# Optimization experiments

Measured on AMD Instinct MI355X. Metric: run time of the kernel, lower is better.

Reference implementation:

```python
import jax, jax.numpy as jnp
import numpy as np

K = 5
TAU = 0.5
N = 8192
IN_DIM = 128
OUT_DIM = 128


def setup_inputs() -> dict:
    key = jax.random.key(0)
    k1, k2, k3 = jax.random.split(key, 3)
    x = jax.random.normal(k1, (N, IN_DIM), dtype=jnp.float32)
    laplacian = jax.random.normal(k2, (N, N), dtype=jnp.float32) / np.sqrt(N)
    # xavier-uniform-like init for theta (K, in_dim, out_dim)
    limit = np.sqrt(6.0 / (IN_DIM + OUT_DIM))
    theta = jax.random.uniform(k3, (K, IN_DIM, OUT_DIM), dtype=jnp.float32,
                               minval=-limit, maxval=limit)
    return {"x": x, "laplacian": laplacian, "theta": theta}


def _cheb_coeff(k_order: int, tau: float) -> jnp.ndarray:
    # c_k = (2/K) * exp(-tau * cos(pi*(k+0.5)/K)), Chebyshev-Gauss nodes
    ks = jnp.arange(k_order, dtype=jnp.float32)
    x_k = jnp.cos(jnp.pi * (ks + 0.5) / k_order)
    return (2.0 / k_order) * jnp.exp(-tau * x_k)


def reference(x, laplacian, theta):
    coeff = _cheb_coeff(K, TAU)  # (K,)
    # Chebyshev recurrence: T_0 = x, T_1 = L x, T_k = 2 L T_{k-1} - T_{k-2}
    tx_prev, tx_curr = x, laplacian @ x
    tx_list = [tx_prev, tx_curr]
    for _ in range(2, K):
        tx_next = 2.0 * (laplacian @ tx_curr) - tx_prev
        tx_list.append(tx_next)
        tx_prev, tx_curr = tx_curr, tx_next
    tx_stack = jnp.stack(tx_list, axis=0)  # (K, N, in_dim)
    return jnp.einsum('kni,kio,k->no', tx_stack, theta, coeff)
```

## Files before the change

### kernel.cpp

```cpp
#include <hip/hip_runtime.h>
#include <hip/hip_bf16.h>
#include <cmath>

#define NROWS 8192
#define DIM   128
#define KDIM  8192
#define BM    32
#define BN    128
#define BK    64
#define SPLITK 4
#define KCHUNK (KDIM / SPLITK)
#define GITERS (KCHUNK / BK)
#define MTILES (NROWS / BM)
#define LDSTRIDE 80

typedef __bf16 bf16_t;
typedef __bf16 bf16x8 __attribute__((ext_vector_type(8)));
typedef float  f32x4  __attribute__((ext_vector_type(4)));

__device__ __forceinline__ void async16(const void* g, void* l) {
    __builtin_amdgcn_global_load_lds(
        (const __attribute__((address_space(1))) unsigned int*)g,
        (__attribute__((address_space(3))) unsigned int*)l, 16, 0, 0);
}

__global__ void k_theta(const float* __restrict__ th, bf16_t* __restrict__ out,
                        float c0, float c1, float c2, float c3, float c4) {
    int idx = blockIdx.x * 256 + threadIdx.x;
    int k = idx >> 14;
    int o = (idx >> 7) & 127;
    int i = idx & 127;
    float c = (k == 0) ? c0 : (k == 1) ? c1 : (k == 2) ? c2 : (k == 3) ? c3 : c4;
    out[idx] = (bf16_t)(c * th[(k << 14) + (i << 7) + o]);
}

template <int MODE>
__global__ __launch_bounds__(256, 4)
void k_gemm(const void* __restrict__ Ap, const bf16_t* __restrict__ Bt,
            float* __restrict__ partial, bf16_t* __restrict__ Lbf_out) {
    __shared__ __align__(16) bf16_t As[2][BM * BK];
    __shared__ __align__(16) bf16_t Bs[2][BN * BK];

    const int t     = threadIdx.x;
    const int mTile = blockIdx.x & (MTILES - 1);
    const int s     = blockIdx.x >> 8;
    const int mb    = mTile * BM;
    const int k0base = s * KCHUNK;
    const int wave = t >> 6, lane = t & 63;
    const int wM = (wave & 1) * 16;
    const int wN = (wave >> 1) * 64;
    const int lm = lane & 15, lk = lane >> 4;
    const int lrow = lane >> 3;
    const int lsrc = (lane & 7) ^ lrow;
    const int rA   = wave * 8 + lrow;

    f32x4 acc[4];
#pragma unroll
    for (int b = 0; b < 4; ++b) acc[b] = (f32x4)0.0f;

    float4 RA[2][2];

    auto stageB = [&](int kk, int buf) {
        const int k0 = k0base + kk * BK;
#pragma unroll
        for (int i = 0; i < 4; ++i) {
            const int n = wave * 32 + i * 8 + lrow;
            async16(Bt + (size_t)n * KDIM + k0 + lsrc * 8,
                    &Bs[buf][(wave * 32 + i * 8) * BK]);
        }
    };
    auto stageA0 = [&](int kk, int buf) {
        const int k0 = k0base + kk * BK;
        async16((const bf16_t*)Ap + (size_t)(mb + rA) * KDIM + k0 + lsrc * 8,
                &As[buf][wave * 8 * BK]);
    };
    auto loadA2 = [&](int kk, int p) {
        const int k0 = k0base + kk * BK;
        const float* base = (const float*)Ap + (size_t)(mb + rA) * KDIM + k0 + lsrc * 8;
        RA[p][0] = *(const float4*)base;
        RA[p][1] = *(const float4*)(base + 4);
    };
    auto writeA2 = [&](int kk, int buf, int p) {
        bf16x8 v;
        v[0] = (bf16_t)RA[p][0].x; v[1] = (bf16_t)RA[p][0].y;
        v[2] = (bf16_t)RA[p][0].z; v[3] = (bf16_t)RA[p][0].w;
        v[4] = (bf16_t)RA[p][1].x; v[5] = (bf16_t)RA[p][1].y;
        v[6] = (bf16_t)RA[p][1].z; v[7] = (bf16_t)RA[p][1].w;
        *(bf16x8*)(&As[buf][rA * BK + (lane & 7) * 8]) = v;
        const int k0 = k0base + kk * BK;
        *(bf16x8*)(Lbf_out + (size_t)(mb + rA) * KDIM + k0 + lsrc * 8) = v;
    };

    auto compute = [&](int buf) {
#pragma unroll
        for (int ko = 0; ko < 2; ++ko) {
            const int csX = (ko * 4 + lk) ^ (lm & 7);
            bf16x8 af = *(const bf16x8*)(&As[buf][(wM + lm) * BK + csX * 8]);
            bf16x8 bfr[4];
#pragma unroll
            for (int tn = 0; tn < 4; ++tn)
                bfr[tn] = *(const bf16x8*)(&Bs[buf][(wN + tn * 16 + lm) * BK + csX * 8]);
#pragma unroll
            for (int tn = 0; tn < 4; ++tn)
                acc[tn] = __builtin_amdgcn_mfma_f32_16x16x32_bf16(
                    af, bfr[tn], acc[tn], 0, 0, 0);
        }
    };

    if (MODE == 0) {
        stageA0(0, 0); stageB(0, 0);
        for (int kk = 0; kk < GITERS; ++kk) {
            const int buf = kk & 1;
            __syncthreads();
            if (kk + 1 < GITERS) { stageA0(kk + 1, buf ^ 1); stageB(kk + 1, buf ^ 1); }
            compute(buf);
        }
    } else {
        loadA2(0, 0); stageB(0, 0);
        for (int kk = 0; kk < GITERS; ++kk) {
            const int buf = kk & 1;
            writeA2(kk, buf, kk & 1);
            __syncthreads();
            if (kk + 1 < GITERS) { loadA2(kk + 1, (kk + 1) & 1); stageB(kk + 1, buf ^ 1); }
            compute(buf);
        }
    }

    float* pOut = partial + (size_t)s * NROWS * DIM;
#pragma unroll
    for (int tn = 0; tn < 4; ++tn)
#pragma unroll
        for (int r = 0; r < 4; ++r) {
            const int row = mb + wM + lk * 4 + r;
            const int col = wN + tn * 16 + lm;
            pOut[(size_t)row * DIM + col] = acc[tn][r];
        }
}

template <int MODE>
__global__ void k_combine(const float* __restrict__ src, const float* __restrict__ prev,
                          float* __restrict__ f32dst, bf16_t* __restrict__ tbf,
                          bf16_t* __restrict__ bt) {
    __shared__ bf16_t tl[128 * 24];
    const size_t S = (size_t)NROWS * DIM;
    const int t  = threadIdx.x;
    const int n0 = blockIdx.x * 16;
    const int nl = t >> 4;
    const int dp = (t & 15) * 8;
    const int n  = n0 + nl;

    float y[8];
    if (MODE == 0) {
        float4 a = *(const float4*)(src + (size_t)n * DIM + dp);
        float4 b = *(const float4*)(src + (size_t)n * DIM + dp + 4);
        y[0] = a.x; y[1] = a.y; y[2] = a.z; y[3] = a.w;
        y[4] = b.x; y[5] = b.y; y[6] = b.z; y[7] = b.w;
    } else {
#pragma unroll
        for (int j = 0; j < 8; ++j) y[j] = 0.0f;
#pragma unroll
        for (int ss = 0; ss < SPLITK; ++ss) {
            const float* p = src + (size_t)ss * S + (size_t)n * DIM + dp;
            float4 a = *(const float4*)p;
            float4 b = *(const float4*)(p + 4);
            y[0] += a.x; y[1] += a.y; y[2] += a.z; y[3] += a.w;
            y[4] += b.x; y[5] += b.y; y[6] += b.z; y[7] += b.w;
        }
        if (MODE == 2) {
            float4 a = *(const float4*)(prev + (size_t)n * DIM + dp);
            float4 b = *(const float4*)(prev + (size_t)n * DIM + dp + 4);
            y[0] = 2.0f * y[0] - a.x; y[1] = 2.0f * y[1] - a.y;
            y[2] = 2.0f * y[2] - a.z; y[3] = 2.0f * y[3] - a.w;
            y[4] = 2.0f * y[4] - b.x; y[5] = 2.0f * y[5] - b.y;
            y[6] = 2.0f * y[6] - b.z; y[7] = 2.0f * y[7] - b.w;
        }
    }
    if (f32dst) {
        float4 a, b;
        a.x = y[0]; a.y = y[1]; a.z = y[2]; a.w = y[3];
        b.x = y[4]; b.y = y[5]; b.z = y[6]; b.w = y[7];
        *(float4*)(f32dst + (size_t)n * DIM + dp) = a;
        *(float4*)(f32dst + (size_t)n * DIM + dp + 4) = b;
    }
    bf16x8 v;
#pragma unroll
    for (int j = 0; j < 8; ++j) v[j] = (bf16_t)y[j];
    *(bf16x8*)(tbf + (size_t)n * DIM + dp) = v;
    if (bt) {
#pragma unroll
        for (int j = 0; j < 8; ++j) tl[(dp + j) * 24 + nl] = v[j];
        __syncthreads();
        const int d = t >> 1, h = (t & 1) * 8;
        bf16x8 w = *(const bf16x8*)(&tl[d * 24 + h]);
        *(bf16x8*)(bt + (size_t)d * NROWS + n0 + h) = w;
    }
}

__global__ __launch_bounds__(256, 2)
void k_proj(const bf16_t* __restrict__ T, const bf16_t* __restrict__ W,
            float* __restrict__ out) {
    __shared__ __align__(16) bf16_t As[64 * LDSTRIDE];
    __shared__ __align__(16) bf16_t Bs[128 * LDSTRIDE];

    const int t  = threadIdx.x;
    const int mb = blockIdx.x * 64;
    const int wave = t >> 6, lane = t & 63;
    const int wM = (wave & 1) * 32;
    const int wN = (wave >> 1) * 64;
    const int lm = lane & 15, lk = lane >> 4;
    const int arow = t >> 3;
    const int asc  = t & 7;
    const size_t S = (size_t)NROWS * DIM;

    f32x4 acc[2][4];
#pragma unroll
    for (int a = 0; a < 2; ++a)
#pragma unroll
        for (int b = 0; b < 4; ++b) acc[a][b] = (f32x4)0.0f;

    bf16x8 aR[2], bR[4];

    auto loadT = [&](int it) {
        const int seg = it >> 1;
        const int h   = (it & 1) * 64;
#pragma unroll
        for (int rep = 0; rep < 2; ++rep) {
            const int r = rep * 32 + arow;
            aR[rep] = *(const bf16x8*)(T + (size_t)seg * S +
                        (size_t)(mb + r) * DIM + h + asc * 8);
        }
#pragma unroll
        for (int rep = 0; rep < 4; ++rep) {
            const int o = rep * 32 + arow;
            bR[rep] = *(const bf16x8*)(W + seg * 16384 + o * 128 + h + asc * 8);
        }
    };
    auto storeT = [&]() {
#pragma unroll
        for (int rep = 0; rep < 2; ++rep) {
            const int r = rep * 32 + arow;
            *(bf16x8*)(&As[r * LDSTRIDE + asc * 8]) = aR[rep];
        }
#pragma unroll
        for (int rep = 0; rep < 4; ++rep) {
            const int o = rep * 32 + arow;
            *(bf16x8*)(&Bs[o * LDSTRIDE + asc * 8]) = bR[rep];
        }
    };

    loadT(0);
    for (int it = 0; it < 10; ++it) {
        __syncthreads();
        storeT();
        __syncthreads();
        if (it + 1 < 10) loadT(it + 1);
#pragma unroll
        for (int ko = 0; ko < 2; ++ko) {
            bf16x8 af[2], bfr[4];
#pragma unroll
            for (int tm = 0; tm < 2; ++tm)
                af[tm] = *(const bf16x8*)(&As[(wM + tm * 16 + lm) * LDSTRIDE +
                                              (ko * 4 + lk) * 8]);
#pragma unroll
            for (int tn = 0; tn < 4; ++tn)
                bfr[tn] = *(const bf16x8*)(&Bs[(wN + tn * 16 + lm) * LDSTRIDE +
                                               (ko * 4 + lk) * 8]);
#pragma unroll
            for (int tm = 0; tm < 2; ++tm)
#pragma unroll
                for (int tn = 0; tn < 4; ++tn)
                    acc[tm][tn] = __builtin_amdgcn_mfma_f32_16x16x32_bf16(
                        af[tm], bfr[tn], acc[tm][tn], 0, 0, 0);
        }
    }
#pragma unroll
    for (int tm = 0; tm < 2; ++tm)
#pragma unroll
        for (int tn = 0; tn < 4; ++tn)
#pragma unroll
            for (int r = 0; r < 4; ++r) {
                const int row = mb + wM + tm * 16 + lk * 4 + r;
                const int col = wN + tn * 16 + lm;
                out[(size_t)row * DIM + col] = acc[tm][tn][r];
            }
}

extern "C" void kernel_launch(void* const* d_in, const int* in_sizes, int n_in,
                              void* d_out, int out_size, void* d_ws, size_t ws_size,
                              hipStream_t stream) {
    const float* x  = nullptr;
    const float* L  = nullptr;
    const float* th = nullptr;
    for (int i = 0; i < n_in; ++i) {
        if (in_sizes[i] == NROWS * KDIM)       L  = (const float*)d_in[i];
        else if (in_sizes[i] == NROWS * DIM)   x  = (const float*)d_in[i];
        else if (in_sizes[i] == 5 * DIM * DIM) th = (const float*)d_in[i];
    }
    float* out = (float*)d_out;

    const size_t S = (size_t)NROWS * DIM;
    char* ws = (char*)d_ws;
    size_t off = 0;
    auto alloc = [&](size_t bytes) {
        void* p = ws + off;
        off = (off + bytes + 255) & ~(size_t)255;
        return p;
    };
    bf16_t* Tbf     = (bf16_t*)alloc(5 * S * 2);
    bf16_t* Bt      = (bf16_t*)alloc(5 * S * 2);
    float*  Tf32    = (float*)alloc(2 * S * 4);
    bf16_t* thT     = (bf16_t*)alloc(5 * 128 * 128 * 2);
    float*  partial = (float*)alloc((size_t)SPLITK * S * 4);
    bf16_t* Lbf     = (bf16_t*)alloc((size_t)NROWS * KDIM * 2);
    if (off > ws_size) return;

    float c[5];
    for (int k = 0; k < 5; ++k)
        c[k] = (float)((2.0 / 5.0) * exp(-0.5 * cos(M_PI * (k + 0.5) / 5.0)));

    dim3 blk(256);
    k_theta<<<320, blk, 0, stream>>>(th, thT, c[0], c[1], c[2], c[3], c[4]);
    k_combine<0><<<512, blk, 0, stream>>>(x, nullptr, nullptr, Tbf, Bt);

    for (int j = 1; j <= 4; ++j) {
        const bf16_t* Bj = Bt + (size_t)(j - 1) * S;
        if (j == 1)
            k_gemm<2><<<MTILES * SPLITK, blk, 0, stream>>>(L, Bj, partial, Lbf);
        else
            k_gemm<0><<<MTILES * SPLITK, blk, 0, stream>>>(Lbf, Bj, partial, nullptr);
        bf16_t* tbf = Tbf + (size_t)j * S;
        bf16_t* bt  = (j < 4) ? Bt + (size_t)j * S : nullptr;
        if (j == 1)
            k_combine<1><<<512, blk, 0, stream>>>(partial, nullptr, Tf32 + S, tbf, bt);
        else if (j == 2)
            k_combine<2><<<512, blk, 0, stream>>>(partial, x, Tf32, tbf, bt);
        else if (j == 3)
            k_combine<2><<<512, blk, 0, stream>>>(partial, Tf32 + S, Tf32 + S, tbf, bt);
        else
            k_combine<2><<<512, blk, 0, stream>>>(partial, Tf32, nullptr, tbf, nullptr);
    }
    k_proj<<<128, blk, 0, stream>>>(Tbf, thT, out);
}
```

Before: 631.8 us.

## Double GEMM M-tile and pre-swizzle bf16 operands into LDS-ready block layout

```diff
diff --git a/kernel.cpp b/kernel.cpp
--- a/kernel.cpp
+++ b/kernel.cpp
@@ -5,18 +5,20 @@
 #define NROWS 8192
 #define DIM   128
 #define KDIM  8192
-#define BM    32
+#define BM    64
 #define BN    128
 #define BK    64
 #define SPLITK 4
 #define KCHUNK (KDIM / SPLITK)
 #define GITERS (KCHUNK / BK)
 #define MTILES (NROWS / BM)
+#define KBLKS  (KDIM / BK)
 #define LDSTRIDE 80
 
 typedef __bf16 bf16_t;
 typedef __bf16 bf16x8 __attribute__((ext_vector_type(8)));
 typedef float  f32x4  __attribute__((ext_vector_type(4)));
+
 
 __device__ __forceinline__ void async16(const void* g, void* l) {
     __builtin_amdgcn_global_load_lds(
@@ -35,7 +37,7 @@
 }
 
 template <int MODE>
-__global__ __launch_bounds__(256, 4)
+__global__ __launch_bounds__(256, 2)
 void k_gemm(const void* __restrict__ Ap, const bf16_t* __restrict__ Bt,
             float* __restrict__ partial, bf16_t* __restrict__ Lbf_out) {
     __shared__ __align__(16) bf16_t As[2][BM * BK];
@@ -43,77 +45,97 @@
 
     const int t     = threadIdx.x;
     const int mTile = blockIdx.x & (MTILES - 1);
-    const int s     = blockIdx.x >> 8;
+    const int s     = blockIdx.x >> 7;
     const int mb    = mTile * BM;
-    const int k0base = s * KCHUNK;
+    const int sKB   = s * (KCHUNK / BK);
+    const int rgA   = mb >> 3;
     const int wave = t >> 6, lane = t & 63;
-    const int wM = (wave & 1) * 16;
+    const int wM = (wave & 1) * 32;
     const int wN = (wave >> 1) * 64;
     const int lm = lane & 15, lk = lane >> 4;
     const int lrow = lane >> 3;
-    const int lsrc = (lane & 7) ^ lrow;
-    const int rA   = wave * 8 + lrow;
-
-    f32x4 acc[4];
-#pragma unroll
-    for (int b = 0; b < 4; ++b) acc[b] = (f32x4)0.0f;
-
-    float4 RA[2][2];
+    const int p0   = lane & 7;
+    const int lsrc = p0 ^ lrow;
+
+    f32x4 acc[2][4];
+#pragma unroll
+    for (int a = 0; a < 2; ++a)
+#pragma unroll
+        for (int b = 0; b < 4; ++b) acc[a][b] = (f32x4)0.0f;
+
+    float4 RA[2][2][2];
 
     auto stageB = [&](int kk, int buf) {
-        const int k0 = k0base + kk * BK;
+        const int kblk = sKB + kk;
 #pragma unroll
         for (int i = 0; i < 4; ++i) {
-            const int n = wave * 32 + i * 8 + lrow;
-            async16(Bt + (size_t)n * KDIM + k0 + lsrc * 8,
+            const int fg = wave * 4 + i;
+            async16(Bt + (((size_t)fg * KBLKS + kblk) * 64 + lane) * 8,
                     &Bs[buf][(wave * 32 + i * 8) * BK]);
         }
     };
     auto stageA0 = [&](int kk, int buf) {
-        const int k0 = k0base + kk * BK;
-        async16((const bf16_t*)Ap + (size_t)(mb + rA) * KDIM + k0 + lsrc * 8,
-                &As[buf][wave * 8 * BK]);
-    };
-    auto loadA2 = [&](int kk, int p) {
-        const int k0 = k0base + kk * BK;
-        const float* base = (const float*)Ap + (size_t)(mb + rA) * KDIM + k0 + lsrc * 8;
-        RA[p][0] = *(const float4*)base;
-        RA[p][1] = *(const float4*)(base + 4);
-    };
-    auto writeA2 = [&](int kk, int buf, int p) {
-        bf16x8 v;
-        v[0] = (bf16_t)RA[p][0].x; v[1] = (bf16_t)RA[p][0].y;
-        v[2] = (bf16_t)RA[p][0].z; v[3] = (bf16_t)RA[p][0].w;
-        v[4] = (bf16_t)RA[p][1].x; v[5] = (bf16_t)RA[p][1].y;
-        v[6] = (bf16_t)RA[p][1].z; v[7] = (bf16_t)RA[p][1].w;
-        *(bf16x8*)(&As[buf][rA * BK + (lane & 7) * 8]) = v;
-        const int k0 = k0base + kk * BK;
-        *(bf16x8*)(Lbf_out + (size_t)(mb + rA) * KDIM + k0 + lsrc * 8) = v;
+        const int kblk = sKB + kk;
+#pragma unroll
+        for (int j = 0; j < 2; ++j) {
+            const int rg = rgA + wave * 2 + j;
+            async16((const bf16_t*)Ap + (((size_t)rg * KBLKS + kblk) * 64 + lane) * 8,
+                    &As[buf][(wave * 16 + j * 8) * BK]);
+        }
+    };
+    auto loadA2 = [&](int kk, int st) {
+        const int k0 = s * KCHUNK + kk * BK;
+#pragma unroll
+        for (int j = 0; j < 2; ++j) {
+            const int row = mb + wave * 16 + j * 8 + lrow;
+            const float* base = (const float*)Ap + (size_t)row * KDIM + k0 + lsrc * 8;
+            RA[st][j][0] = *(const float4*)base;
+            RA[st][j][1] = *(const float4*)(base + 4);
+        }
+    };
+    auto writeA2 = [&](int kk, int buf, int st) {
+        const int kblk = sKB + kk;
+#pragma unroll
+        for (int j = 0; j < 2; ++j) {
+            bf16x8 v;
+            v[0] = (bf16_t)RA[st][j][0].x; v[1] = (bf16_t)RA[st][j][0].y;
+            v[2] = (bf16_t)RA[st][j][0].z; v[3] = (bf16_t)RA[st][j][0].w;
+            v[4] = (bf16_t)RA[st][j][1].x; v[5] = (bf16_t)RA[st][j][1].y;
+            v[6] = (bf16_t)RA[st][j][1].z; v[7] = (bf16_t)RA[st][j][1].w;
+            *(bf16x8*)(&As[buf][(wave * 16 + j * 8 + lrow) * BK + p0 * 8]) = v;
+            const int rg = rgA + wave * 2 + j;
+            *(bf16x8*)(Lbf_out + (((size_t)rg * KBLKS + kblk) * 64 + lane) * 8) = v;
+        }
     };
 
     auto compute = [&](int buf) {
 #pragma unroll
         for (int ko = 0; ko < 2; ++ko) {
             const int csX = (ko * 4 + lk) ^ (lm & 7);
-            bf16x8 af = *(const bf16x8*)(&As[buf][(wM + lm) * BK + csX * 8]);
-            bf16x8 bfr[4];
+            bf16x8 af[2], bfr[4];
+#pragma unroll
+            for (int tm = 0; tm < 2; ++tm)
+                af[tm] = *(const bf16x8*)(&As[buf][(wM + tm * 16 + lm) * BK + csX * 8]);
 #pragma unroll
             for (int tn = 0; tn < 4; ++tn)
                 bfr[tn] = *(const bf16x8*)(&Bs[buf][(wN + tn * 16 + lm) * BK + csX * 8]);
 #pragma unroll
-            for (int tn = 0; tn < 4; ++tn)
-                acc[tn] = __builtin_amdgcn_mfma_f32_16x16x32_bf16(
-                    af, bfr[tn], acc[tn], 0, 0, 0);
+            for (int tm = 0; tm < 2; ++tm)
+#pragma unroll
+                for (int tn = 0; tn < 4; ++tn)
+                    acc[tm][tn] = __builtin_amdgcn_mfma_f32_16x16x32_bf16(
+                        af[tm], bfr[tn], acc[tm][tn], 0, 0, 0);
         }
     };
 
     if (MODE == 0) {
         stageA0(0, 0); stageB(0, 0);
+        __syncthreads();
         for (int kk = 0; kk < GITERS; ++kk) {
             const int buf = kk & 1;
-            __syncthreads();
             if (kk + 1 < GITERS) { stageA0(kk + 1, buf ^ 1); stageB(kk + 1, buf ^ 1); }
             compute(buf);
+            __syncthreads();
         }
     } else {
         loadA2(0, 0); stageB(0, 0);
@@ -128,13 +150,15 @@
 
     float* pOut = partial + (size_t)s * NROWS * DIM;
 #pragma unroll
-    for (int tn = 0; tn < 4; ++tn)
-#pragma unroll
-        for (int r = 0; r < 4; ++r) {
-            const int row = mb + wM + lk * 4 + r;
-            const int col = wN + tn * 16 + lm;
-            pOut[(size_t)row * DIM + col] = acc[tn][r];
-        }
+    for (int tm = 0; tm < 2; ++tm)
+#pragma unroll
+        for (int tn = 0; tn < 4; ++tn)
+#pragma unroll
+            for (int r = 0; r < 4; ++r) {
+                const int row = mb + wM + tm * 16 + lk * 4 + r;
+                const int col = wN + tn * 16 + lm;
+                pOut[(size_t)row * DIM + col] = acc[tm][tn][r];
+            }
 }
 
 template <int MODE>
@@ -190,9 +214,13 @@
 #pragma unroll
         for (int j = 0; j < 8; ++j) tl[(dp + j) * 24 + nl] = v[j];
         __syncthreads();
-        const int d = t >> 1, h = (t & 1) * 8;
+        const int d = t >> 1;
+        const int h = (t & 1) * 8;
         bf16x8 w = *(const bf16x8*)(&tl[d * 24 + h]);
-        *(bf16x8*)(bt + (size_t)d * NROWS + n0 + h) = w;
+        const int c    = ((n0 + h) >> 3) & 7;
+        const int lane = (d & 7) * 8 + (c ^ (d & 7));
+        const size_t a16 = ((size_t)(d >> 3) * KBLKS + (n0 >> 6)) * 64 + lane;
+        *(bf16x8*)(bt + a16 * 8) = w;
     }
 }
 
```

After: 591.5 us. -6.4%, faster.
